# Kernel tuning notes

Hardware: AMD Instinct MI355X
Metric: run time of the kernel (lower is better)

Reference implementation:

```python
import jax, jax.numpy as jnp
import numpy as np

BN_EPS = 1e-5
DIST_MIN = 1e-8
K = 3


def setup_inputs() -> dict:
    key = jax.random.key(0)
    ks = jax.random.split(key, 6)
    B, Nl, Nh, Ch, Cl, out_ch = 4, 8192, 2048, 256, 128, 256
    in_ch = Ch + Cl
    xyz_low = jax.random.normal(ks[0], (B, Nl, 3), jnp.float32)
    xyz_high = jax.random.normal(ks[1], (B, Nh, 3), jnp.float32)
    feat_low = jax.random.normal(ks[2], (B, Cl, Nl), jnp.float32)
    feat_high = jax.random.normal(ks[3], (B, Ch, Nh), jnp.float32)
    # 1x1 Conv1d params (kernel size 1 -> plain channel-mixing matrix)
    W = jax.random.normal(ks[4], (out_ch, in_ch), jnp.float32) * (1.0 / np.sqrt(in_ch))
    b = jax.random.normal(ks[5], (out_ch,), jnp.float32) * 0.01
    gamma = jnp.ones((out_ch,), jnp.float32)
    beta = jnp.zeros((out_ch,), jnp.float32)
    return {"xyz_low": xyz_low, "xyz_high": xyz_high, "feat_low": feat_low,
            "feat_high": feat_high, "W": W, "b": b, "gamma": gamma, "beta": beta}


def reference(xyz_low, xyz_high, feat_low, feat_high, W, b, gamma, beta):
    # --- pairwise euclidean distances (B, Nl, Nh), like torch.cdist ---
    d2 = (jnp.sum(xyz_low ** 2, -1)[:, :, None]
          + jnp.sum(xyz_high ** 2, -1)[:, None, :]
          - 2.0 * jnp.einsum('bld,bhd->blh', xyz_low, xyz_high))
    d = jnp.sqrt(jnp.maximum(d2, 0.0))
    # --- 3-NN (smallest distances) ---
    _, idx = jax.lax.top_k(-d, K)                      # (B, Nl, K)
    dist = jnp.maximum(jnp.take_along_axis(d, idx, axis=-1), DIST_MIN)
    w = 1.0 / dist
    w = w / jnp.sum(w, axis=-1, keepdims=True)         # (B, Nl, K)
    # --- gather neighbor features and inverse-distance interpolate ---
    f_high_T = jnp.transpose(feat_high, (0, 2, 1))      # (B, Nh, Ch)
    neigh = jax.vmap(lambda f, i: f[i])(f_high_T, idx)  # (B, Nl, K, Ch)
    f_interp = jnp.einsum('blk,blkc->bcl', w, neigh)    # (B, Ch, Nl)
    f_cat = jnp.concatenate([f_interp, feat_low], axis=1)  # (B, Ch+Cl, Nl)
    # --- 1x1 Conv1d + BatchNorm1d (training-mode batch stats) + ReLU ---
    y = jnp.einsum('oc,bcn->bon', W, f_cat) + b[None, :, None]
    mean = jnp.mean(y, axis=(0, 2), keepdims=True)
    var = jnp.var(y, axis=(0, 2), keepdims=True)        # biased, as in torch BN
    yn = (y - mean) * jax.lax.rsqrt(var + BN_EPS)
    return jax.nn.relu(gamma[None, :, None] * yn + beta[None, :, None])
```

## Files before the change

kernel.cpp:

```cpp
#include <hip/hip_runtime.h>

constexpr int B_   = 4;
constexpr int NL   = 8192;
constexpr int NH   = 2048;
constexpr int CH   = 256;
constexpr int CL   = 128;
constexpr int CIN  = 384;
constexpr int COUT = 256;

typedef _Float16 f16;
typedef _Float16 f16x8 __attribute__((ext_vector_type(8)));
typedef float    f32x4 __attribute__((ext_vector_type(4)));

#define INS3F(d, h, B0, B1, B2, I0, I1, I2) do {                             \
    bool c0_ = (d) < (B0), c1_ = (d) < (B1), c2_ = (d) < (B2);               \
    int ni1_ = c0_ ? (I0) : (c1_ ? (h) : (I1));                              \
    int ni2_ = c1_ ? (I1) : (c2_ ? (h) : (I2));                              \
    I0 = c0_ ? (h) : (I0); I1 = ni1_; I2 = ni2_;                             \
    float nb1_ = __builtin_amdgcn_fmed3f(B0, B1, (d));                       \
    float nb2_ = __builtin_amdgcn_fmed3f(B1, B2, (d));                       \
    B0 = fminf(B0, (d)); B1 = nb1_; B2 = nb2_;                               \
} while (0)

__global__ __launch_bounds__(256) void prep_kernel(
    const float* __restrict__ feat_high, const float* __restrict__ Wm,
    f16* __restrict__ fhT, f16* __restrict__ Wh)
{
    __shared__ float tt[32][33];
    const int bid = blockIdx.x, tid = threadIdx.x;

    if (bid < 512) {
        const int tx = tid & 31, ty = tid >> 5;
        #pragma unroll
        for (int k = 0; k < 4; ++k) {
            const int u  = bid * 4 + k;
            const int ub = u >> 9, ut = u & 511;
            const int h0 = (ut & 63) * 32, c0 = (ut >> 6) * 32;
            #pragma unroll
            for (int pp = 0; pp < 4; ++pp)
                tt[ty + pp * 8][tx] =
                    feat_high[((size_t)ub * CH + c0 + ty + pp * 8) * NH + h0 + tx];
            __syncthreads();
            #pragma unroll
            for (int pp = 0; pp < 4; ++pp)
                fhT[((size_t)ub * NH + h0 + ty + pp * 8) * CH + c0 + tx] =
                    (f16)tt[tx][ty + pp * 8];
            __syncthreads();
        }
    } else {
        const int i = (bid - 512) * 256 + tid;
        Wh[i] = (f16)Wm[i];
    }
}

__global__ __launch_bounds__(1024, 8) void gemm_kernel(
    const float* __restrict__ xyz_low, const float* __restrict__ xyz_high,
    const float* __restrict__ feat_low, const f16* __restrict__ fhT,
    const f16* __restrict__ Wh, const float* __restrict__ bias,
    f16* __restrict__ yh, float* __restrict__ ps, float* __restrict__ psq)
{
    __shared__ __align__(16) char smraw[53120];
    f16*            As   = (f16*)smraw;
    float4*         pts  = (float4*)smraw;
    float*          md   = (float*)(smraw + 32768);
    unsigned short* mi   = (unsigned short*)(smraw + 45312);
    int*            idxL = (int*)(smraw + 51584);
    float*          wL   = (float*)(smraw + 52352);

    const int bid = blockIdx.x, tid = threadIdx.x;
    const int b = bid >> 7, l0 = (bid & 127) * 64;
    const int lane = tid & 63, w = tid >> 6;

    {
        const float* xh = xyz_high + (size_t)b * NH * 3;
        #pragma unroll
        for (int k = 0; k < 2; ++k) {
            const int h = k * 1024 + tid;
            float x = xh[h * 3], yy = xh[h * 3 + 1], z = xh[h * 3 + 2];
            pts[h] = make_float4(x, yy, z, x * x + yy * yy + z * z);
        }
    }
    __syncthreads();
    {
        const float* xl = xyz_low + ((size_t)b * NL + l0 + lane) * 3;
        const float lx = xl[0], ly = xl[1], lz = xl[2];
        const float sl = lx * lx + ly * ly + lz * lz;

        float a0 = 1e30f, a1 = 1e30f, a2 = 1e30f;
        int ia0 = 0, ia1 = 0, ia2 = 0;
        const int h0 = w * 128;
        #pragma unroll 8
        for (int i = 0; i < 128; ++i) {
            float4 pA = pts[h0 + i];
            float dA = fmaf(-2.0f, fmaf(lx, pA.x, fmaf(ly, pA.y, lz * pA.z)),
                            sl + pA.w);
            INS3F(dA, h0 + i, a0, a1, a2, ia0, ia1, ia2);
        }
        const int cb = lane * 49 + w * 3;
        md[cb] = a0;     mi[cb] = (unsigned short)ia0;
        md[cb + 1] = a1; mi[cb + 1] = (unsigned short)ia1;
        md[cb + 2] = a2; mi[cb + 2] = (unsigned short)ia2;
    }
    __syncthreads();

    if (tid < 64) {
        float e0 = 1e30f, e1 = 1e30f, e2 = 1e30f;
        int j0 = 0, j1 = 0, j2 = 0;
        #pragma unroll
        for (int q = 0; q < 48; ++q) {
            float d = md[tid * 49 + q];
            int  ii = mi[tid * 49 + q];
            INS3F(d, ii, e0, e1, e2, j0, j1, j2);
        }
        float d0 = sqrtf(fmaxf(e0, 0.0f));
        float d1 = sqrtf(fmaxf(e1, 0.0f));
        float d2f = sqrtf(fmaxf(e2, 0.0f));
        float iw0 = 1.0f / fmaxf(d0, 1e-8f);
        float iw1 = 1.0f / fmaxf(d1, 1e-8f);
        float iw2 = 1.0f / fmaxf(d2f, 1e-8f);
        float sum = iw0 + iw1 + iw2;
        idxL[tid] = j0; idxL[64 + tid] = j1; idxL[128 + tid] = j2;
        wL[tid] = iw0 / sum; wL[64 + tid] = iw1 / sum; wL[128 + tid] = iw2 / sum;
    }
    __syncthreads();

    {
        const int p = tid >> 4, q = tid & 15;
        const int j0 = idxL[p], j1 = idxL[64 + p], j2 = idxL[128 + p];
        const float u0 = wL[p], u1 = wL[64 + p], u2 = wL[128 + p];
        const f16* r0 = fhT + ((size_t)b * NH + j0) * CH + q * 16;
        const f16* r1 = fhT + ((size_t)b * NH + j1) * CH + q * 16;
        const f16* r2 = fhT + ((size_t)b * NH + j2) * CH + q * 16;
        #pragma unroll
        for (int j = 0; j < 2; ++j) {
            f16x8 v0 = *(const f16x8*)(r0 + j * 8);
            f16x8 v1 = *(const f16x8*)(r1 + j * 8);
            f16x8 v2 = *(const f16x8*)(r2 + j * 8);
            f16x8 o;
            #pragma unroll
            for (int e = 0; e < 8; ++e)
                o[e] = (f16)(u0 * (float)v0[e] + u1 * (float)v1[e]
                             + u2 * (float)v2[e]);
            *(f16x8*)&As[p * 392 + q * 16 + j * 8] = o;
        }
        const int l = tid & 63, cq = tid >> 6;
        const float* flb = feat_low + ((size_t)b * CL + cq * 8) * NL + l0 + l;
        f16 tmp[8];
        #pragma unroll
        for (int i = 0; i < 8; ++i)
            tmp[i] = (f16)flb[(size_t)i * NL];
        *(f16x8*)&As[l * 392 + 256 + cq * 8] = *(const f16x8*)&tmp[0];
    }
    __syncthreads();

    f32x4 acc[4] = {};
    const int kb = (lane >> 4) * 8;
    const int r  = lane & 15;
    #pragma unroll
    for (int kt = 0; kt < 12; ++kt) {
        const int k0 = kt * 32;
        f16x8 a = *(const f16x8*)&Wh[(size_t)(w * 16 + r) * CIN + k0 + kb];
        f16x8 bb[4];
        #pragma unroll
        for (int ni = 0; ni < 4; ++ni)
            bb[ni] = *(const f16x8*)&As[(ni * 16 + r) * 392 + k0 + kb];
        #pragma unroll
        for (int ni = 0; ni < 4; ++ni)
            acc[ni] = __builtin_amdgcn_mfma_f32_16x16x32_f16(
                a, bb[ni], acc[ni], 0, 0, 0);
    }

    const int r4 = (lane >> 4) * 4, cl = lane & 15;
    #pragma unroll
    for (int j = 0; j < 4; ++j) {
        const int o = w * 16 + r4 + j;
        const float bi = bias[o];
        float s = 0.0f, sq = 0.0f;
        #pragma unroll
        for (int ni = 0; ni < 4; ++ni) {
            acc[ni][j] += bi;
            float v = acc[ni][j];
            s += v; sq += v * v;
        }
        #pragma unroll
        for (int m = 1; m < 16; m <<= 1) {
            s  += __shfl_xor(s, m);
            sq += __shfl_xor(sq, m);
        }
        if (cl == 0) {
            ps [o * 512 + bid] = s;
            psq[o * 512 + bid] = sq;
        }
    }
    __syncthreads();

    f16* Ys = (f16*)smraw;
    #pragma unroll
    for (int j = 0; j < 4; ++j) {
        const int o = w * 16 + r4 + j;
        #pragma unroll
        for (int ni = 0; ni < 4; ++ni)
            Ys[o * 72 + cl + ni * 16] = (f16)acc[ni][j];
    }
    __syncthreads();
    {
        const int o = tid >> 2, qtr = tid & 3;
        f16* dst = yh + ((size_t)b * COUT + o) * NL + l0 + qtr * 16;
        *(f16x8*)(dst)     = *(const f16x8*)&Ys[o * 72 + qtr * 16];
        *(f16x8*)(dst + 8) = *(const f16x8*)&Ys[o * 72 + qtr * 16 + 8];
    }
}

__global__ __launch_bounds__(256) void stats_apply_kernel(
    const float* __restrict__ ps, const float* __restrict__ psq,
    const f16* __restrict__ yh,
    const float* __restrict__ gamma, const float* __restrict__ beta,
    float* __restrict__ y)
{
    const int o = blockIdx.x, b = blockIdx.y, tid = threadIdx.x;
    const int w = tid >> 6, lane = tid & 63;

    float s = ps[o * 512 + tid] + ps[o * 512 + 256 + tid];
    float q = psq[o * 512 + tid] + psq[o * 512 + 256 + tid];
    #pragma unroll
    for (int m = 32; m > 0; m >>= 1) {
        s += __shfl_down(s, m);
        q += __shfl_down(q, m);
    }
    __shared__ float red[8];
    if (lane == 0) { red[w] = s; red[4 + w] = q; }
    __syncthreads();
    s = red[0] + red[1] + red[2] + red[3];
    q = red[4] + red[5] + red[6] + red[7];
    const float n  = (float)(B_ * NL);
    const float mu = s / n;
    const float rs = rsqrtf(q / n - mu * mu + 1e-5f);
    const float g  = gamma[o], be = beta[o];

    const f16* src = yh + ((size_t)b * COUT + o) * NL;
    float*     dst = y  + ((size_t)b * COUT + o) * NL;
    #pragma unroll
    for (int it = 0; it < 4; ++it) {
        const int base = it * 2048 + tid * 8;
        f16x8 v = *(const f16x8*)(src + base);
        float4 o1, o2;
        o1.x = fmaxf(fmaf(g, ((float)v[0] - mu) * rs, be), 0.0f);
        o1.y = fmaxf(fmaf(g, ((float)v[1] - mu) * rs, be), 0.0f);
        o1.z = fmaxf(fmaf(g, ((float)v[2] - mu) * rs, be), 0.0f);
        o1.w = fmaxf(fmaf(g, ((float)v[3] - mu) * rs, be), 0.0f);
        o2.x = fmaxf(fmaf(g, ((float)v[4] - mu) * rs, be), 0.0f);
        o2.y = fmaxf(fmaf(g, ((float)v[5] - mu) * rs, be), 0.0f);
        o2.z = fmaxf(fmaf(g, ((float)v[6] - mu) * rs, be), 0.0f);
        o2.w = fmaxf(fmaf(g, ((float)v[7] - mu) * rs, be), 0.0f);
        *(float4*)(dst + base)     = o1;
        *(float4*)(dst + base + 4) = o2;
    }
}

extern "C" void kernel_launch(void* const* d_in, const int* in_sizes, int n_in,
                              void* d_out, int out_size, void* d_ws, size_t ws_size,
                              hipStream_t stream)
{
    const float* xyz_low   = (const float*)d_in[0];
    const float* xyz_high  = (const float*)d_in[1];
    const float* feat_low  = (const float*)d_in[2];
    const float* feat_high = (const float*)d_in[3];
    const float* Wm        = (const float*)d_in[4];
    const float* bias      = (const float*)d_in[5];
    const float* gamma     = (const float*)d_in[6];
    const float* beta      = (const float*)d_in[7];
    float* y = (float*)d_out;

    float* ps   = (float*)d_ws;
    float* psq  = ps + (size_t)COUT * 512;
    f16*   Wh   = (f16*)(psq + (size_t)COUT * 512);
    f16*   fhT  = Wh + (size_t)COUT * CIN;
    f16*   yh   = fhT + (size_t)B_ * NH * CH;

    prep_kernel<<<896, 256, 0, stream>>>(feat_high, Wm, fhT, Wh);
    gemm_kernel<<<512, 1024, 0, stream>>>(
        xyz_low, xyz_high, feat_low, fhT, Wh, bias, yh, ps, psq);
    stats_apply_kernel<<<dim3(COUT, B_), 256, 0, stream>>>(
        ps, psq, yh, gamma, beta, y);
}
```

Before: 66.98 us.

## Process 128 low points per block to reuse each loaded high point twice

Each block now handles 128 low-resolution points instead of 64. Every thread scans the high points against two query points, so each shared-memory point load is reused. The GEMM and stats stage runs twice per block over 64-point halves, and the grid drops from 512 to 256 blocks. This trades fewer blocks and more registers (launch bounds relaxed) for less shared-memory traffic and less duplicated xyz_high staging, but 256 blocks may leave some of the 256 CUs underused.

```diff
diff --git a/kernel.cpp b/kernel.cpp
--- a/kernel.cpp
+++ b/kernel.cpp
@@ -53,22 +53,22 @@
     }
 }
 
-__global__ __launch_bounds__(1024, 8) void gemm_kernel(
+__global__ __launch_bounds__(1024, 4) void gemm_kernel(
     const float* __restrict__ xyz_low, const float* __restrict__ xyz_high,
     const float* __restrict__ feat_low, const f16* __restrict__ fhT,
     const f16* __restrict__ Wh, const float* __restrict__ bias,
     f16* __restrict__ yh, float* __restrict__ ps, float* __restrict__ psq)
 {
-    __shared__ __align__(16) char smraw[53120];
+    __shared__ __align__(16) char smraw[53248];
     f16*            As   = (f16*)smraw;
     float4*         pts  = (float4*)smraw;
-    float*          md   = (float*)(smraw + 32768);
-    unsigned short* mi   = (unsigned short*)(smraw + 45312);
-    int*            idxL = (int*)(smraw + 51584);
-    float*          wL   = (float*)(smraw + 52352);
+    float*          md   = (float*)smraw;
+    unsigned short* mi   = (unsigned short*)(smraw + 25088);
+    int*            idxL = (int*)(smraw + 50176);
+    float*          wL   = (float*)(smraw + 51712);
 
     const int bid = blockIdx.x, tid = threadIdx.x;
-    const int b = bid >> 7, l0 = (bid & 127) * 64;
+    const int b = bid >> 6, l0 = (bid & 63) * 128;
     const int lane = tid & 63, w = tid >> 6;
 
     {
@@ -81,29 +81,43 @@
         }
     }
     __syncthreads();
+    float a0 = 1e30f, a1 = 1e30f, a2 = 1e30f;
+    float c0 = 1e30f, c1 = 1e30f, c2 = 1e30f;
+    int ia0 = 0, ia1 = 0, ia2 = 0, ic0 = 0, ic1 = 0, ic2 = 0;
     {
-        const float* xl = xyz_low + ((size_t)b * NL + l0 + lane) * 3;
-        const float lx = xl[0], ly = xl[1], lz = xl[2];
-        const float sl = lx * lx + ly * ly + lz * lz;
-
-        float a0 = 1e30f, a1 = 1e30f, a2 = 1e30f;
-        int ia0 = 0, ia1 = 0, ia2 = 0;
+        const float* xlA = xyz_low + ((size_t)b * NL + l0 + lane) * 3;
+        const float* xlB = xyz_low + ((size_t)b * NL + l0 + 64 + lane) * 3;
+        const float lxA = xlA[0], lyA = xlA[1], lzA = xlA[2];
+        const float lxB = xlB[0], lyB = xlB[1], lzB = xlB[2];
+        const float slA = lxA * lxA + lyA * lyA + lzA * lzA;
+        const float slB = lxB * lxB + lyB * lyB + lzB * lzB;
+
         const int h0 = w * 128;
         #pragma unroll 8
         for (int i = 0; i < 128; ++i) {
-            float4 pA = pts[h0 + i];
-            float dA = fmaf(-2.0f, fmaf(lx, pA.x, fmaf(ly, pA.y, lz * pA.z)),
-                            sl + pA.w);
+            float4 pt = pts[h0 + i];
+            float dA = fmaf(-2.0f, fmaf(lxA, pt.x, fmaf(lyA, pt.y, lzA * pt.z)),
+                            slA + pt.w);
+            float dB = fmaf(-2.0f, fmaf(lxB, pt.x, fmaf(lyB, pt.y, lzB * pt.z)),
+                            slB + pt.w);
             INS3F(dA, h0 + i, a0, a1, a2, ia0, ia1, ia2);
-        }
-        const int cb = lane * 49 + w * 3;
-        md[cb] = a0;     mi[cb] = (unsigned short)ia0;
-        md[cb + 1] = a1; mi[cb + 1] = (unsigned short)ia1;
-        md[cb + 2] = a2; mi[cb + 2] = (unsigned short)ia2;
-    }
-    __syncthreads();
-
-    if (tid < 64) {
+            INS3F(dB, h0 + i, c0, c1, c2, ic0, ic1, ic2);
+        }
+    }
+    __syncthreads();
+    {
+        const int cbA = lane * 49 + w * 3;
+        const int cbB = (64 + lane) * 49 + w * 3;
+        md[cbA] = a0;     mi[cbA] = (unsigned short)ia0;
+        md[cbA + 1] = a1; mi[cbA + 1] = (unsigned short)ia1;
+        md[cbA + 2] = a2; mi[cbA + 2] = (unsigned short)ia2;
+        md[cbB] = c0;     mi[cbB] = (unsigned short)ic0;
+        md[cbB + 1] = c1; mi[cbB + 1] = (unsigned short)ic1;
+        md[cbB + 2] = c2; mi[cbB + 2] = (unsigned short)ic2;
+    }
+    __syncthreads();
+
+    if (tid < 128) {
         float e0 = 1e30f, e1 = 1e30f, e2 = 1e30f;
         int j0 = 0, j1 = 0, j2 = 0;
         #pragma unroll
@@ -119,95 +133,103 @@
         float iw1 = 1.0f / fmaxf(d1, 1e-8f);
         float iw2 = 1.0f / fmaxf(d2f, 1e-8f);
         float sum = iw0 + iw1 + iw2;
-        idxL[tid] = j0; idxL[64 + tid] = j1; idxL[128 + tid] = j2;
-        wL[tid] = iw0 / sum; wL[64 + tid] = iw1 / sum; wL[128 + tid] = iw2 / sum;
-    }
-    __syncthreads();
-
-    {
-        const int p = tid >> 4, q = tid & 15;
-        const int j0 = idxL[p], j1 = idxL[64 + p], j2 = idxL[128 + p];
-        const float u0 = wL[p], u1 = wL[64 + p], u2 = wL[128 + p];
-        const f16* r0 = fhT + ((size_t)b * NH + j0) * CH + q * 16;
-        const f16* r1 = fhT + ((size_t)b * NH + j1) * CH + q * 16;
-        const f16* r2 = fhT + ((size_t)b * NH + j2) * CH + q * 16;
-        #pragma unroll
-        for (int j = 0; j < 2; ++j) {
-            f16x8 v0 = *(const f16x8*)(r0 + j * 8);
-            f16x8 v1 = *(const f16x8*)(r1 + j * 8);
-            f16x8 v2 = *(const f16x8*)(r2 + j * 8);
-            f16x8 o;
-            #pragma unroll
-            for (int e = 0; e < 8; ++e)
-                o[e] = (f16)(u0 * (float)v0[e] + u1 * (float)v1[e]
-                             + u2 * (float)v2[e]);
-            *(f16x8*)&As[p * 392 + q * 16 + j * 8] = o;
-        }
-        const int l = tid & 63, cq = tid >> 6;
-        const float* flb = feat_low + ((size_t)b * CL + cq * 8) * NL + l0 + l;
-        f16 tmp[8];
-        #pragma unroll
-        for (int i = 0; i < 8; ++i)
-            tmp[i] = (f16)flb[(size_t)i * NL];
-        *(f16x8*)&As[l * 392 + 256 + cq * 8] = *(const f16x8*)&tmp[0];
-    }
-    __syncthreads();
-
-    f32x4 acc[4] = {};
+        idxL[tid] = j0; idxL[128 + tid] = j1; idxL[256 + tid] = j2;
+        wL[tid] = iw0 / sum; wL[128 + tid] = iw1 / sum; wL[256 + tid] = iw2 / sum;
+    }
+    __syncthreads();
+
     const int kb = (lane >> 4) * 8;
     const int r  = lane & 15;
+    const int r4 = (lane >> 4) * 4, cl = lane & 15;
+
     #pragma unroll
-    for (int kt = 0; kt < 12; ++kt) {
-        const int k0 = kt * 32;
-        f16x8 a = *(const f16x8*)&Wh[(size_t)(w * 16 + r) * CIN + k0 + kb];
-        f16x8 bb[4];
-        #pragma unroll
-        for (int ni = 0; ni < 4; ++ni)
-            bb[ni] = *(const f16x8*)&As[(ni * 16 + r) * 392 + k0 + kb];
-        #pragma unroll
-        for (int ni = 0; ni < 4; ++ni)
-            acc[ni] = __builtin_amdgcn_mfma_f32_16x16x32_f16(
-                a, bb[ni], acc[ni], 0, 0, 0);
-    }
-
-    const int r4 = (lane >> 4) * 4, cl = lane & 15;
-    #pragma unroll
-    for (int j = 0; j < 4; ++j) {
-        const int o = w * 16 + r4 + j;
-        const float bi = bias[o];
-        float s = 0.0f, sq = 0.0f;
-        #pragma unroll
-        for (int ni = 0; ni < 4; ++ni) {
-            acc[ni][j] += bi;
-            float v = acc[ni][j];
-            s += v; sq += v * v;
-        }
-        #pragma unroll
-        for (int m = 1; m < 16; m <<= 1) {
-            s  += __shfl_xor(s, m);
-            sq += __shfl_xor(sq, m);
-        }
-        if (cl == 0) {
-            ps [o * 512 + bid] = s;
-            psq[o * 512 + bid] = sq;
-        }
-    }
-    __syncthreads();
-
-    f16* Ys = (f16*)smraw;
-    #pragma unroll
-    for (int j = 0; j < 4; ++j) {
-        const int o = w * 16 + r4 + j;
-        #pragma unroll
-        for (int ni = 0; ni < 4; ++ni)
-            Ys[o * 72 + cl + ni * 16] = (f16)acc[ni][j];
-    }
-    __syncthreads();
-    {
-        const int o = tid >> 2, qtr = tid & 3;
-        f16* dst = yh + ((size_t)b * COUT + o) * NL + l0 + qtr * 16;
-        *(f16x8*)(dst)     = *(const f16x8*)&Ys[o * 72 + qtr * 16];
-        *(f16x8*)(dst + 8) = *(const f16x8*)&Ys[o * 72 + qtr * 16 + 8];
+    for (int half = 0; half < 2; ++half) {
+        const int l0h = l0 + half * 64;
+
+        {
+            const int p = tid >> 4, q = tid & 15;
+            const int lp = half * 64 + p;
+            const int j0 = idxL[lp], j1 = idxL[128 + lp], j2 = idxL[256 + lp];
+            const float u0 = wL[lp], u1 = wL[128 + lp], u2 = wL[256 + lp];
+            const f16* r0 = fhT + ((size_t)b * NH + j0) * CH + q * 16;
+            const f16* r1 = fhT + ((size_t)b * NH + j1) * CH + q * 16;
+            const f16* r2 = fhT + ((size_t)b * NH + j2) * CH + q * 16;
+            #pragma unroll
+            for (int j = 0; j < 2; ++j) {
+                f16x8 v0 = *(const f16x8*)(r0 + j * 8);
+                f16x8 v1 = *(const f16x8*)(r1 + j * 8);
+                f16x8 v2 = *(const f16x8*)(r2 + j * 8);
+                f16x8 o;
+                #pragma unroll
+                for (int e = 0; e < 8; ++e)
+                    o[e] = (f16)(u0 * (float)v0[e] + u1 * (float)v1[e]
+                                 + u2 * (float)v2[e]);
+                *(f16x8*)&As[p * 392 + q * 16 + j * 8] = o;
+            }
+            const int l = tid & 63, cq = tid >> 6;
+            const float* flb = feat_low + ((size_t)b * CL + cq * 8) * NL + l0h + l;
+            f16 tmp[8];
+            #pragma unroll
+            for (int i = 0; i < 8; ++i)
+                tmp[i] = (f16)flb[(size_t)i * NL];
+            *(f16x8*)&As[l * 392 + 256 + cq * 8] = *(const f16x8*)&tmp[0];
+        }
+        __syncthreads();
+
+        f32x4 acc[4] = {};
+        #pragma unroll
+        for (int kt = 0; kt < 12; ++kt) {
+            const int k0 = kt * 32;
+            f16x8 a = *(const f16x8*)&Wh[(size_t)(w * 16 + r) * CIN + k0 + kb];
+            f16x8 bb[4];
+            #pragma unroll
+            for (int ni = 0; ni < 4; ++ni)
+                bb[ni] = *(const f16x8*)&As[(ni * 16 + r) * 392 + k0 + kb];
+            #pragma unroll
+            for (int ni = 0; ni < 4; ++ni)
+                acc[ni] = __builtin_amdgcn_mfma_f32_16x16x32_f16(
+                    a, bb[ni], acc[ni], 0, 0, 0);
+        }
+
+        #pragma unroll
+        for (int j = 0; j < 4; ++j) {
+            const int o = w * 16 + r4 + j;
+            const float bi = bias[o];
+            float s = 0.0f, sq = 0.0f;
+            #pragma unroll
+            for (int ni = 0; ni < 4; ++ni) {
+                acc[ni][j] += bi;
+                float v = acc[ni][j];
+                s += v; sq += v * v;
+            }
+            #pragma unroll
+            for (int m = 1; m < 16; m <<= 1) {
+                s  += __shfl_xor(s, m);
+                sq += __shfl_xor(sq, m);
+            }
+            if (cl == 0) {
+                ps [o * 512 + bid * 2 + half] = s;
+                psq[o * 512 + bid * 2 + half] = sq;
+            }
+        }
+        __syncthreads();
+
+        f16* Ys = (f16*)smraw;
+        #pragma unroll
+        for (int j = 0; j < 4; ++j) {
+            const int o = w * 16 + r4 + j;
+            #pragma unroll
+            for (int ni = 0; ni < 4; ++ni)
+                Ys[o * 72 + cl + ni * 16] = (f16)acc[ni][j];
+        }
+        __syncthreads();
+        {
+            const int o = tid >> 2, qtr = tid & 3;
+            f16* dst = yh + ((size_t)b * COUT + o) * NL + l0h + qtr * 16;
+            *(f16x8*)(dst)     = *(const f16x8*)&Ys[o * 72 + qtr * 16];
+            *(f16x8*)(dst + 8) = *(const f16x8*)&Ys[o * 72 + qtr * 16 + 8];
+        }
+        __syncthreads();
     }
 }
 
@@ -278,7 +300,7 @@
     f16*   yh   = fhT + (size_t)B_ * NH * CH;
 
     prep_kernel<<<896, 256, 0, stream>>>(feat_high, Wm, fhT, Wh);
-    gemm_kernel<<<512, 1024, 0, stream>>>(
+    gemm_kernel<<<256, 1024, 0, stream>>>(
         xyz_low, xyz_high, feat_low, fhT, Wh, bias, yh, ps, psq);
     stats_apply_kernel<<<dim3(COUT, B_), 256, 0, stream>>>(
         ps, psq, yh, gamma, beta, y);
```

Result: slower. 81.19 us (+21.2%).
